# Performance work log

Hardware: AMD Instinct MI355X
Metric: run time of the kernel (lower is better)

The kernel has to match this reference:

```python
import jax, jax.numpy as jnp
import numpy as np
import math

RADIUS = 32
NUM_HEADS = 8

B, L, DIM = 2, 8192, 256


def setup_inputs() -> dict:
    key = jax.random.key(0)
    k1, k2, k3, k4, k5 = jax.random.split(key, 5)
    s_in = 1.0 / math.sqrt(DIM)
    return {
        "x": jax.random.normal(k1, (B, L, DIM), dtype=jnp.float32),
        "w_qkv": jax.random.normal(k2, (DIM, 3 * DIM), dtype=jnp.float32) * s_in,
        "b_qkv": jax.random.normal(k3, (3 * DIM,), dtype=jnp.float32) * 0.01,
        "w_proj": jax.random.normal(k4, (DIM, DIM), dtype=jnp.float32) * s_in,
        "b_proj": jax.random.normal(k5, (DIM,), dtype=jnp.float32) * 0.01,
    }


def reference(x, w_qkv, b_qkv, w_proj, b_proj):
    B, L, dim = x.shape
    H = NUM_HEADS
    hd = dim // H
    R = RADIUS
    W = 2 * R + 1
    scale = math.sqrt(hd)

    qkv = x @ w_qkv + b_qkv                      # (B, L, 3*dim)
    qkv = qkv.reshape(B, L, 3, H, hd)
    qkv = jnp.transpose(qkv, (2, 0, 3, 1, 4))    # (3, B, H, L, hd)
    q = qkv[0].reshape(B * H, L, hd)
    k = qkv[1].reshape(B * H, L, hd)
    v = qkv[2].reshape(B * H, L, hd)

    # zero-pad along sequence (matches F.pad value=0: boundary windows attend
    # to zero vectors with logit 0, included in softmax)
    k_p = jnp.pad(k, ((0, 0), (R, R), (0, 0)))   # (BH, L+2R, hd)
    v_p = jnp.pad(v, ((0, 0), (R, R), (0, 0)))

    idx = jnp.arange(L)[:, None] + jnp.arange(W)[None, :]  # (L, W)
    k_w = k_p[:, idx]                            # (BH, L, W, hd)
    v_w = v_p[:, idx]                            # (BH, L, W, hd)

    scores = jnp.einsum('bld,blwd->blw', q, k_w) / scale
    attn = jax.nn.softmax(scores, axis=-1)
    out = jnp.einsum('blw,blwd->bld', attn, v_w)  # (BH, L, hd)

    out = out.reshape(B, H, L, hd)
    out = jnp.transpose(out, (0, 2, 1, 3)).reshape(B, L, dim)
    return out @ w_proj + b_proj
```

## Files before the change

### kernel.cpp

```cpp
#include <hip/hip_runtime.h>
#include <hip/hip_bf16.h>
#include <math.h>

#define B_SZ 2
#define L_SZ 8192
#define DIM 256
#define H_N 8
#define HD 32
#define RAD 32
#define W_SZ 65
#define M_ROWS (B_SZ * L_SZ)

typedef __bf16 bf16x8 __attribute__((ext_vector_type(8)));
typedef float  f32x4  __attribute__((ext_vector_type(4)));

typedef const __attribute__((address_space(1))) void gvoid_t;
typedef __attribute__((address_space(3))) void lvoid_t;

__global__ __launch_bounds__(256) void prep(const float* __restrict__ x,
                                            const float* __restrict__ wq,
                                            const float* __restrict__ wp,
                                            __bf16* __restrict__ xb,
                                            __bf16* __restrict__ wqT,
                                            __bf16* __restrict__ wpT) {
    int idx = blockIdx.x * 256 + threadIdx.x;
    const int N1 = M_ROWS * DIM / 4;
    const int N2 = 3 * DIM * DIM;
    if (idx < N1) {
        float4 v = reinterpret_cast<const float4*>(x)[idx];
        __bf16* o = xb + (size_t)idx * 4;
        o[0] = (__bf16)v.x; o[1] = (__bf16)v.y; o[2] = (__bf16)v.z; o[3] = (__bf16)v.w;
    } else if (idx < N1 + N2) {
        int i2 = idx - N1;
        int n = i2 >> 8, k = i2 & 255;
        wqT[i2] = (__bf16)wq[(size_t)k * (3 * DIM) + n];
    } else {
        int i3 = idx - N1 - N2;
        int n = i3 >> 8, k = i3 & 255;
        wpT[i3] = (__bf16)wp[(size_t)k * DIM + n];
    }
}

template<int BM, int BN, int WM, int WN, int N_DIM, int K_DIM, bool OUT_BF16>
__global__ __launch_bounds__(256) void gemm_bt(const __bf16* __restrict__ A,
                                               const __bf16* __restrict__ BT,
                                               const float* __restrict__ bias,
                                               void* __restrict__ Cout) {
    constexpr int BK = 32;
    constexpr int FM = BM / WM / 16;
    constexpr int FN = BN / WN / 16;
    __shared__ __bf16 As[BM * BK];
    __shared__ __bf16 Bs[BN * BK];
    const int tid = threadIdx.x;
    const int lane = tid & 63;
    const int wave = tid >> 6;
    const int wr = wave / WN;
    const int wc = wave % WN;
    const int row0 = blockIdx.y * BM;
    const int col0 = blockIdx.x * BN;

    f32x4 acc[FM][FN] = {};

    const int fr = lane & 15;
    const int fg = lane >> 4;

    for (int k0 = 0; k0 < K_DIM; k0 += BK) {
        #pragma unroll
        for (int i = 0; i < BM / 64; ++i) {
            int c  = tid + i * 256;
            int r  = c >> 2;
            int kk = (c & 3) * 8;
            __builtin_amdgcn_global_load_lds(
                (gvoid_t*)(A + (size_t)(row0 + r) * K_DIM + (k0 + kk)),
                (lvoid_t*)(As + c * 8), 16, 0, 0);
        }
        #pragma unroll
        for (int i = 0; i < BN / 64; ++i) {
            int c  = tid + i * 256;
            int r  = c >> 2;
            int kk = (c & 3) * 8;
            __builtin_amdgcn_global_load_lds(
                (gvoid_t*)(BT + (size_t)(col0 + r) * K_DIM + (k0 + kk)),
                (lvoid_t*)(Bs + c * 8), 16, 0, 0);
        }
        asm volatile("s_waitcnt vmcnt(0)" ::: "memory");
        __syncthreads();

        bf16x8 a[FM], b[FN];
        #pragma unroll
        for (int i = 0; i < FM; ++i)
            a[i] = *reinterpret_cast<const bf16x8*>(&As[(wr * (BM / WM) + i * 16 + fr) * BK + fg * 8]);
        #pragma unroll
        for (int j = 0; j < FN; ++j)
            b[j] = *reinterpret_cast<const bf16x8*>(&Bs[(wc * (BN / WN) + j * 16 + fr) * BK + fg * 8]);
        #pragma unroll
        for (int i = 0; i < FM; ++i)
            #pragma unroll
            for (int j = 0; j < FN; ++j)
                acc[i][j] = __builtin_amdgcn_mfma_f32_16x16x32_bf16(a[i], b[j], acc[i][j], 0, 0, 0);
        __syncthreads();
    }

    #pragma unroll
    for (int i = 0; i < FM; ++i) {
        #pragma unroll
        for (int j = 0; j < FN; ++j) {
            int cc = col0 + wc * (BN / WN) + j * 16 + fr;
            float bv = bias[cc];
            #pragma unroll
            for (int r = 0; r < 4; ++r) {
                int rr = row0 + wr * (BM / WM) + i * 16 + fg * 4 + r;
                float v = acc[i][j][r] + bv;
                if (OUT_BF16)
                    ((__bf16*)Cout)[(size_t)rr * N_DIM + cc] = (__bf16)v;
                else
                    ((float*)Cout)[(size_t)rr * N_DIM + cc] = v;
            }
        }
    }
}

__global__ __launch_bounds__(256) void natt_mfma(const __bf16* __restrict__ qkv,
                                                 __bf16* __restrict__ attn_out) {
    constexpr int VS = 216;
    __shared__ __bf16 vsT[32 * VS];
    __shared__ __bf16 plds[4][16 * 104];

    const int tid  = threadIdx.x;
    const int lane = tid & 63;
    const int wave = tid >> 6;
    const int l15  = lane & 15;
    const int fg   = lane >> 4;
    const int bh = blockIdx.y;
    const int b  = bh >> 3;
    const int h  = bh & 7;
    const int bq0 = blockIdx.x * 128;
    const int wq0 = bq0 + wave * 32;

    const __bf16* base = qkv + (size_t)b * L_SZ * 768 + h * 32;

    if (tid < 96) {
        int d = tid / 3, part = tid % 3;
        *reinterpret_cast<bf16x8*>(&vsT[d * VS + 192 + part * 8]) = bf16x8{};
    }
    if (lane < 48) {
        int r = lane / 3, part = lane % 3;
        *reinterpret_cast<bf16x8*>(&plds[wave][r * 104 + 80 + part * 8]) = bf16x8{};
    }

    #pragma unroll
    for (int i = 0; i < 3; ++i) {
        int c  = tid + i * 256;
        int sp = c >> 2;
        int dq = c & 3;
        int kp = bq0 - 32 + sp;
        bf16x8 v = {};
        if (kp >= 0 && kp < L_SZ)
            v = *reinterpret_cast<const bf16x8*>(base + (size_t)kp * 768 + 512 + dq * 8);
        int g = (sp >> 3) ^ dq;
        #pragma unroll
        for (int j = 0; j < 8; ++j)
            vsT[(dq * 8 + j) * VS + g * 8 + (sp & 7)] = v[j];
    }

    bf16x8 kf[6];
    #pragma unroll
    for (int t = 0; t < 6; ++t) {
        int kp = wq0 - 32 + t * 16 + l15;
        bf16x8 kv = {};
        if (kp >= 0 && kp < L_SZ)
            kv = *reinterpret_cast<const bf16x8*>(base + (size_t)kp * 768 + 256 + fg * 8);
        kf[t] = kv;
    }
    bf16x8 qf[2];
    #pragma unroll
    for (int s = 0; s < 2; ++s)
        qf[s] = *reinterpret_cast<const bf16x8*>(base + (size_t)(wq0 + s * 16 + l15) * 768 + fg * 8);

    __syncthreads();

    const float rscale = 0.17677669529663687f;
    __bf16* pw = plds[wave];

    #pragma unroll
    for (int s = 0; s < 2; ++s) {
        f32x4 st[5];
        __builtin_amdgcn_s_setprio(1);
        #pragma unroll
        for (int t2 = 0; t2 < 5; ++t2)
            st[t2] = __builtin_amdgcn_mfma_f32_16x16x32_bf16(qf[s], kf[s + t2], f32x4{}, 0, 0, 0);
        __builtin_amdgcn_s_setprio(0);

        float pvl[5][4], inv[4];
        #pragma unroll
        for (int r = 0; r < 4; ++r) {
            const int qr = fg * 4 + r;
            float sum = 0.f;
            #pragma unroll
            for (int t2 = 0; t2 < 5; ++t2) {
                int pr = t2 * 16 + l15;
                bool valid = (pr >= qr) && (pr <= qr + 64);
                float e = valid ? __expf(st[t2][r] * rscale) : 0.f;
                pvl[t2][r] = e;
                sum += e;
            }
            #pragma unroll
            for (int x = 1; x <= 8; x <<= 1) sum += __shfl_xor(sum, x);
            inv[r] = 1.f / sum;
        }

        #pragma unroll
        for (int t2 = 0; t2 < 5; ++t2)
            #pragma unroll
            for (int r = 0; r < 4; ++r)
                pw[(fg * 4 + r) * 104 + t2 * 16 + l15] = (__bf16)pvl[t2][r];

        f32x4 acc[2] = {};
        #pragma unroll
        for (int ks = 0; ks < 3; ++ks) {
            bf16x8 pf = *reinterpret_cast<const bf16x8*>(&pw[l15 * 104 + ks * 32 + fg * 8]);
            __builtin_amdgcn_s_setprio(1);
            #pragma unroll
            for (int dt = 0; dt < 2; ++dt) {
                int d = dt * 16 + l15;
                int g = (4 * wave + 2 * s + 4 * ks + fg) ^ ((d >> 3) & 3);
                bf16x8 vf = *reinterpret_cast<const bf16x8*>(&vsT[d * VS + g * 8]);
                acc[dt] = __builtin_amdgcn_mfma_f32_16x16x32_bf16(pf, vf, acc[dt], 0, 0, 0);
            }
            __builtin_amdgcn_s_setprio(0);
        }

        __bf16* outp = attn_out + ((size_t)(b * L_SZ + wq0 + s * 16)) * 256 + h * 32;
        #pragma unroll
        for (int dt = 0; dt < 2; ++dt)
            #pragma unroll
            for (int r = 0; r < 4; ++r)
                outp[(size_t)(fg * 4 + r) * 256 + dt * 16 + l15] = (__bf16)(acc[dt][r] * inv[r]);
    }
}

extern "C" void kernel_launch(void* const* d_in, const int* in_sizes, int n_in,
                              void* d_out, int out_size, void* d_ws, size_t ws_size,
                              hipStream_t stream) {
    const float* x      = (const float*)d_in[0];
    const float* w_qkv  = (const float*)d_in[1];
    const float* b_qkv  = (const float*)d_in[2];
    const float* w_proj = (const float*)d_in[3];
    const float* b_proj = (const float*)d_in[4];
    float* out = (float*)d_out;

    __bf16* xb     = (__bf16*)d_ws;
    __bf16* wqkvT  = xb    + (size_t)M_ROWS * DIM;
    __bf16* wprojT = wqkvT + (size_t)(3 * DIM) * DIM;
    __bf16* qkvb   = wprojT + (size_t)DIM * DIM;
    __bf16* ab     = qkvb  + (size_t)M_ROWS * (3 * DIM);

    prep<<<5120, 256, 0, stream>>>(x, w_qkv, w_proj, xb, wqkvT, wprojT);

    dim3 g1(3 * DIM / 128, M_ROWS / 128);
    gemm_bt<128, 128, 2, 2, 3 * DIM, DIM, true><<<g1, 256, 0, stream>>>(xb, wqkvT, b_qkv, qkvb);

    dim3 g2(L_SZ / 128, B_SZ * H_N);
    natt_mfma<<<g2, 256, 0, stream>>>(qkvb, ab);

    dim3 g3(DIM / 128, M_ROWS / 64);
    gemm_bt<64, 128, 1, 4, DIM, DIM, false><<<g3, 256, 0, stream>>>(ab, wprojT, b_proj, out);
}
```

Baseline: 48.24 us.

## Fuse x bf16 cast into QKV GEMM and keep attention probabilities in registers

The fp32-to-bf16 conversion of x moves out of the prep kernel and into the QKV GEMM's A-tile load, so the separate bf16 copy of x is never written to or read back from global memory. In the attention kernel the score MFMA operands are transposed, so each lane holds one query's scores. The normalized probabilities then feed a 16x16x16 bf16 MFMA directly from registers, with no round trip through LDS. This drops the per-wave P scratch buffer and its zero-fill, but the GEMM's A loads become synchronous register loads instead of direct-to-LDS loads, and the P·V step now issues five smaller MFMAs instead of three.

```diff
diff --git a/kernel.cpp b/kernel.cpp
--- a/kernel.cpp
+++ b/kernel.cpp
@@ -8,41 +8,48 @@
 #define H_N 8
 #define HD 32
 #define RAD 32
-#define W_SZ 65
 #define M_ROWS (B_SZ * L_SZ)
 
 typedef __bf16 bf16x8 __attribute__((ext_vector_type(8)));
+typedef __bf16 bf16x4 __attribute__((ext_vector_type(4)));
+typedef short  s16x4  __attribute__((ext_vector_type(4)));
 typedef float  f32x4  __attribute__((ext_vector_type(4)));
 
 typedef const __attribute__((address_space(1))) void gvoid_t;
 typedef __attribute__((address_space(3))) void lvoid_t;
 
-__global__ __launch_bounds__(256) void prep(const float* __restrict__ x,
-                                            const float* __restrict__ wq,
+static __device__ __forceinline__ f32x4 mfma16_bf16(bf16x4 a, bf16x4 b, f32x4 c) {
+#if __has_builtin(__builtin_amdgcn_mfma_f32_16x16x16bf16_1k)
+    return __builtin_amdgcn_mfma_f32_16x16x16bf16_1k(
+        __builtin_bit_cast(s16x4, a), __builtin_bit_cast(s16x4, b), c, 0, 0, 0);
+#elif __has_builtin(__builtin_amdgcn_mfma_f32_16x16x16_bf16)
+    return __builtin_amdgcn_mfma_f32_16x16x16_bf16(a, b, c, 0, 0, 0);
+#else
+    f32x4 d = c;
+    asm volatile("v_mfma_f32_16x16x16_bf16 %0, %1, %2, %0\n\ts_nop 7\n\ts_nop 7"
+                 : "+v"(d) : "v"(a), "v"(b));
+    return d;
+#endif
+}
+
+__global__ __launch_bounds__(256) void prep(const float* __restrict__ wq,
                                             const float* __restrict__ wp,
-                                            __bf16* __restrict__ xb,
                                             __bf16* __restrict__ wqT,
                                             __bf16* __restrict__ wpT) {
     int idx = blockIdx.x * 256 + threadIdx.x;
-    const int N1 = M_ROWS * DIM / 4;
     const int N2 = 3 * DIM * DIM;
-    if (idx < N1) {
-        float4 v = reinterpret_cast<const float4*>(x)[idx];
-        __bf16* o = xb + (size_t)idx * 4;
-        o[0] = (__bf16)v.x; o[1] = (__bf16)v.y; o[2] = (__bf16)v.z; o[3] = (__bf16)v.w;
-    } else if (idx < N1 + N2) {
-        int i2 = idx - N1;
-        int n = i2 >> 8, k = i2 & 255;
-        wqT[i2] = (__bf16)wq[(size_t)k * (3 * DIM) + n];
+    if (idx < N2) {
+        int n = idx >> 8, k = idx & 255;
+        wqT[idx] = (__bf16)wq[(size_t)k * (3 * DIM) + n];
     } else {
-        int i3 = idx - N1 - N2;
+        int i3 = idx - N2;
         int n = i3 >> 8, k = i3 & 255;
         wpT[i3] = (__bf16)wp[(size_t)k * DIM + n];
     }
 }
 
-template<int BM, int BN, int WM, int WN, int N_DIM, int K_DIM, bool OUT_BF16>
-__global__ __launch_bounds__(256) void gemm_bt(const __bf16* __restrict__ A,
+template<int BM, int BN, int WM, int WN, int N_DIM, int K_DIM, bool OUT_BF16, bool CAST_A>
+__global__ __launch_bounds__(256) void gemm_bt(const void* __restrict__ Aptr,
                                                const __bf16* __restrict__ BT,
                                                const float* __restrict__ bias,
                                                void* __restrict__ Cout) {
@@ -66,15 +73,6 @@
 
     for (int k0 = 0; k0 < K_DIM; k0 += BK) {
         #pragma unroll
-        for (int i = 0; i < BM / 64; ++i) {
-            int c  = tid + i * 256;
-            int r  = c >> 2;
-            int kk = (c & 3) * 8;
-            __builtin_amdgcn_global_load_lds(
-                (gvoid_t*)(A + (size_t)(row0 + r) * K_DIM + (k0 + kk)),
-                (lvoid_t*)(As + c * 8), 16, 0, 0);
-        }
-        #pragma unroll
         for (int i = 0; i < BN / 64; ++i) {
             int c  = tid + i * 256;
             int r  = c >> 2;
@@ -83,6 +81,33 @@
                 (gvoid_t*)(BT + (size_t)(col0 + r) * K_DIM + (k0 + kk)),
                 (lvoid_t*)(Bs + c * 8), 16, 0, 0);
         }
+        if (CAST_A) {
+            const float* Af = (const float*)Aptr;
+            #pragma unroll
+            for (int i = 0; i < BM / 64; ++i) {
+                int c  = tid + i * 256;
+                int r  = c >> 2;
+                int kk = (c & 3) * 8;
+                const float* ap = Af + (size_t)(row0 + r) * K_DIM + (k0 + kk);
+                float4 v0 = *reinterpret_cast<const float4*>(ap);
+                float4 v1 = *reinterpret_cast<const float4*>(ap + 4);
+                bf16x8 w;
+                w[0] = (__bf16)v0.x; w[1] = (__bf16)v0.y; w[2] = (__bf16)v0.z; w[3] = (__bf16)v0.w;
+                w[4] = (__bf16)v1.x; w[5] = (__bf16)v1.y; w[6] = (__bf16)v1.z; w[7] = (__bf16)v1.w;
+                *reinterpret_cast<bf16x8*>(As + c * 8) = w;
+            }
+        } else {
+            const __bf16* Ab = (const __bf16*)Aptr;
+            #pragma unroll
+            for (int i = 0; i < BM / 64; ++i) {
+                int c  = tid + i * 256;
+                int r  = c >> 2;
+                int kk = (c & 3) * 8;
+                __builtin_amdgcn_global_load_lds(
+                    (gvoid_t*)(Ab + (size_t)(row0 + r) * K_DIM + (k0 + kk)),
+                    (lvoid_t*)(As + c * 8), 16, 0, 0);
+            }
+        }
         asm volatile("s_waitcnt vmcnt(0)" ::: "memory");
         __syncthreads();
 
@@ -124,7 +149,6 @@
                                                  __bf16* __restrict__ attn_out) {
     constexpr int VS = 216;
     __shared__ __bf16 vsT[32 * VS];
-    __shared__ __bf16 plds[4][16 * 104];
 
     const int tid  = threadIdx.x;
     const int lane = tid & 63;
@@ -139,15 +163,6 @@
 
     const __bf16* base = qkv + (size_t)b * L_SZ * 768 + h * 32;
 
-    if (tid < 96) {
-        int d = tid / 3, part = tid % 3;
-        *reinterpret_cast<bf16x8*>(&vsT[d * VS + 192 + part * 8]) = bf16x8{};
-    }
-    if (lane < 48) {
-        int r = lane / 3, part = lane % 3;
-        *reinterpret_cast<bf16x8*>(&plds[wave][r * 104 + 80 + part * 8]) = bf16x8{};
-    }
-
     #pragma unroll
     for (int i = 0; i < 3; ++i) {
         int c  = tid + i * 256;
@@ -180,62 +195,62 @@
     __syncthreads();
 
     const float rscale = 0.17677669529663687f;
-    __bf16* pw = plds[wave];
 
     #pragma unroll
     for (int s = 0; s < 2; ++s) {
         f32x4 st[5];
         __builtin_amdgcn_s_setprio(1);
         #pragma unroll
-        for (int t2 = 0; t2 < 5; ++t2)
-            st[t2] = __builtin_amdgcn_mfma_f32_16x16x32_bf16(qf[s], kf[s + t2], f32x4{}, 0, 0, 0);
+        for (int t = 0; t < 5; ++t)
+            st[t] = __builtin_amdgcn_mfma_f32_16x16x32_bf16(kf[s + t], qf[s], f32x4{}, 0, 0, 0);
         __builtin_amdgcn_s_setprio(0);
 
-        float pvl[5][4], inv[4];
-        #pragma unroll
-        for (int r = 0; r < 4; ++r) {
-            const int qr = fg * 4 + r;
-            float sum = 0.f;
-            #pragma unroll
-            for (int t2 = 0; t2 < 5; ++t2) {
-                int pr = t2 * 16 + l15;
+        const int qr = l15;
+        float sum = 0.f;
+        #pragma unroll
+        for (int t = 0; t < 5; ++t) {
+            #pragma unroll
+            for (int r = 0; r < 4; ++r) {
+                int pr = 16 * t + 4 * fg + r;
                 bool valid = (pr >= qr) && (pr <= qr + 64);
-                float e = valid ? __expf(st[t2][r] * rscale) : 0.f;
-                pvl[t2][r] = e;
+                float e = valid ? __expf(st[t][r] * rscale) : 0.f;
+                st[t][r] = e;
                 sum += e;
             }
-            #pragma unroll
-            for (int x = 1; x <= 8; x <<= 1) sum += __shfl_xor(sum, x);
-            inv[r] = 1.f / sum;
-        }
-
-        #pragma unroll
-        for (int t2 = 0; t2 < 5; ++t2)
+        }
+        sum += __shfl_xor(sum, 16);
+        sum += __shfl_xor(sum, 32);
+        float inv = 1.f / sum;
+
+        bf16x4 pf[5];
+        #pragma unroll
+        for (int t = 0; t < 5; ++t) {
+            bf16x4 p;
+            #pragma unroll
+            for (int r = 0; r < 4; ++r) p[r] = (__bf16)(st[t][r] * inv);
+            pf[t] = p;
+        }
+
+        f32x4 acc[2] = {};
+        __builtin_amdgcn_s_setprio(1);
+        #pragma unroll
+        for (int c = 0; c < 5; ++c) {
+            #pragma unroll
+            for (int dt = 0; dt < 2; ++dt) {
+                int g = (4 * wave + 2 * s + 2 * c + (fg >> 1)) ^ (2 * dt + (l15 >> 3));
+                bf16x4 vf = *reinterpret_cast<const bf16x4*>(
+                    &vsT[(dt * 16 + l15) * VS + g * 8 + 4 * (fg & 1)]);
+                acc[dt] = mfma16_bf16(pf[c], vf, acc[dt]);
+            }
+        }
+        __builtin_amdgcn_s_setprio(0);
+
+        __bf16* outp = attn_out + ((size_t)(b * L_SZ + wq0 + s * 16)) * 256 + h * 32;
+        #pragma unroll
+        for (int dt = 0; dt < 2; ++dt)
             #pragma unroll
             for (int r = 0; r < 4; ++r)
-                pw[(fg * 4 + r) * 104 + t2 * 16 + l15] = (__bf16)pvl[t2][r];
-
-        f32x4 acc[2] = {};
-        #pragma unroll
-        for (int ks = 0; ks < 3; ++ks) {
-            bf16x8 pf = *reinterpret_cast<const bf16x8*>(&pw[l15 * 104 + ks * 32 + fg * 8]);
-            __builtin_amdgcn_s_setprio(1);
-            #pragma unroll
-            for (int dt = 0; dt < 2; ++dt) {
-                int d = dt * 16 + l15;
-                int g = (4 * wave + 2 * s + 4 * ks + fg) ^ ((d >> 3) & 3);
-                bf16x8 vf = *reinterpret_cast<const bf16x8*>(&vsT[d * VS + g * 8]);
-                acc[dt] = __builtin_amdgcn_mfma_f32_16x16x32_bf16(pf, vf, acc[dt], 0, 0, 0);
-            }
-            __builtin_amdgcn_s_setprio(0);
-        }
-
-        __bf16* outp = attn_out + ((size_t)(b * L_SZ + wq0 + s * 16)) * 256 + h * 32;
-        #pragma unroll
-        for (int dt = 0; dt < 2; ++dt)
-            #pragma unroll
-            for (int r = 0; r < 4; ++r)
-                outp[(size_t)(fg * 4 + r) * 256 + dt * 16 + l15] = (__bf16)(acc[dt][r] * inv[r]);
+                outp[(size_t)(fg * 4 + r) * 256 + dt * 16 + l15] = (__bf16)acc[dt][r];
     }
 }
 
@@ -249,20 +264,19 @@
     const float* b_proj = (const float*)d_in[4];
     float* out = (float*)d_out;
 
-    __bf16* xb     = (__bf16*)d_ws;
-    __bf16* wqkvT  = xb    + (size_t)M_ROWS * DIM;
+    __bf16* wqkvT  = (__bf16*)d_ws;
     __bf16* wprojT = wqkvT + (size_t)(3 * DIM) * DIM;
     __bf16* qkvb   = wprojT + (size_t)DIM * DIM;
     __bf16* ab     = qkvb  + (size_t)M_ROWS * (3 * DIM);
 
-    prep<<<5120, 256, 0, stream>>>(x, w_qkv, w_proj, xb, wqkvT, wprojT);
+    prep<<<1024, 256, 0, stream>>>(w_qkv, w_proj, wqkvT, wprojT);
 
     dim3 g1(3 * DIM / 128, M_ROWS / 128);
-    gemm_bt<128, 128, 2, 2, 3 * DIM, DIM, true><<<g1, 256, 0, stream>>>(xb, wqkvT, b_qkv, qkvb);
+    gemm_bt<128, 128, 2, 2, 3 * DIM, DIM, true, true><<<g1, 256, 0, stream>>>(x, wqkvT, b_qkv, qkvb);
 
     dim3 g2(L_SZ / 128, B_SZ * H_N);
     natt_mfma<<<g2, 256, 0, stream>>>(qkvb, ab);
 
     dim3 g3(DIM / 128, M_ROWS / 64);
-    gemm_bt<64, 128, 1, 4, DIM, DIM, false><<<g3, 256, 0, stream>>>(ab, wprojT, b_proj, out);
-}
+    gemm_bt<64, 128, 1, 4, DIM, DIM, false, false><<<g3, 256, 0, stream>>>(ab, wprojT, b_proj, out);
+}
```

New measurement: 49.73 us. 3.1% more time.
